# Performance work log

Hardware: AMD Instinct MI355X
Metric: run time of the kernel (lower is better)

Reference implementation:

```python
import jax, jax.numpy as jnp
from jax import lax
import numpy as np

D_STATE = 64
BATCH = 64
SEQ_L = 8192


def setup_inputs() -> dict:
    key = jax.random.key(0)
    kx, ka, kb, kc, kd = jax.random.split(key, 5)
    x = jax.random.normal(kx, (BATCH, SEQ_L), dtype=jnp.float32)
    # A = -rand(d_state) - 1.0  -> strictly negative continuous eigenvalues
    A = -jax.random.uniform(ka, (D_STATE,), dtype=jnp.float32) - 1.0
    B = jax.random.normal(kb, (D_STATE, 1), dtype=jnp.float32)
    C = jax.random.normal(kc, (1, D_STATE), dtype=jnp.float32)
    log_delta = jax.random.normal(kd, (1,), dtype=jnp.float32)
    return {"x": x, "A": A, "B": B, "C": C, "log_delta": log_delta}


def reference(x, A, B, C, log_delta):
    batch, L = x.shape
    # --- ZOH discretization ---
    delta = jnp.exp(log_delta)                      # (1,)
    dA = delta * A                                  # (d_state,)  = delta * A
    A_bar = jnp.exp(dA)                             # (d_state,)
    B_bar = ((A_bar - 1.0) / A)[:, None] * B        # (d_state, 1)
    # --- Vandermonde kernel build: K[k] = C @ (A_bar**k * B_bar) ---
    # A_bar**k computed stably as exp(k * delta * A); shape (L, d_state)
    powers = jnp.exp(jnp.arange(L, dtype=x.dtype)[:, None] * dA[None, :])
    K = powers @ (C[0] * B_bar[:, 0])               # (L,)
    # --- Causal convolution: y[t] = sum_{m<=t} K[m] * x[t-m] ---
    # lax.conv is cross-correlation, so the flipped kernel + left padding (L-1)
    # reproduces F.conv1d(x, flip(K), padding=L-1)[..., :L].
    y = lax.conv_general_dilated(
        x[:, None, :],                              # (batch, 1, L)
        K[::-1][None, None, :],                     # (1, 1, L)
        window_strides=(1,),
        padding=[(L - 1, 0)],
        dimension_numbers=("NCH", "OIH", "NCH"),
    )
    return y[:, 0, :]                               # (batch, L)
```

## Files before the change

kernel.cpp:

```cpp
#include <hip/hip_runtime.h>


#define SEQ_L 8192
#define NB    64
#define MCAP  1532
#define XWIN  (1536 + 1024)

__global__ __launch_bounds__(256) void ssm_fir(const float* __restrict__ x,
                                               const float* __restrict__ A,
                                               const float* __restrict__ B,
                                               const float* __restrict__ C,
                                               const float* __restrict__ logd,
                                               float* __restrict__ out)
{
    __shared__ __align__(16) float Kl[1536];
    __shared__ __align__(16) float xL[XWIN];
    __shared__ float sW[64], sDA[64];
    __shared__ int   sM;

    const int tid = threadIdx.x;
    const float delta = __expf(logd[0]);

    if (tid < 64) {
        const float Ad = A[tid];
        const float dA = delta * Ad;
        const float r  = __expf(dA);
        const float w  = C[tid] * (r - 1.f) / Ad * B[tid];
        sW[tid]  = w;
        sDA[tid] = dA;
        float t = fabsf(w) / (1.f - r);
        #pragma unroll
        for (int off = 32; off; off >>= 1) t += __shfl_xor(t, off);
        if (tid == 0) {
            const int M = (int)ceilf((logf(t) + 11.6f) / delta);
            sM = min(max(M, 1), MCAP);
        }
    }
    __syncthreads();
    const int M4 = (sM + 3) & ~3;
    const int H  = (M4 & ~63) + 64;

    for (int mb = tid >> 2; mb < M4; mb += 64) {
        const int d0 = (tid & 3) * 16;
        const float fm = (float)mb;
        float s = 0.f;
        #pragma unroll
        for (int dd = 0; dd < 16; ++dd) {
            const int d = d0 + dd;
            s = fmaf(sW[d], __expf(fm * sDA[d]), s);
        }
        s += __shfl_xor(s, 1);
        s += __shfl_xor(s, 2);
        if ((tid & 3) == 0) Kl[mb] = s;
    }

    const int b  = blockIdx.x >> 3;
    const int t0 = (blockIdx.x & 7) * 1024;
    const float* xb = x + b * SEQ_L;
    const int n4 = (H + 1024) >> 2;
    for (int s4 = tid; s4 < n4; s4 += 256) {
        const int t = t0 - H + s4 * 4;
        float4 v = make_float4(0.f, 0.f, 0.f, 0.f);
        if (t >= 0) v = *(const float4*)(xb + t);
        *(float4*)(xL + s4 * 4) = v;
    }
    __syncthreads();

    const int base = H + tid * 4;
    float4 Wlo = *(const float4*)(xL + base - 4);
    float4 Whi = *(const float4*)(xL + base);
    float a0 = 0.f, a1 = 0.f, a2 = 0.f, a3 = 0.f;
    for (int m0 = 0; m0 < M4; m0 += 4) {
        const float4 Kv = *(const float4*)(Kl + m0);
        a0 = fmaf(Kv.x, Whi.x, a0); a1 = fmaf(Kv.x, Whi.y, a1);
        a2 = fmaf(Kv.x, Whi.z, a2); a3 = fmaf(Kv.x, Whi.w, a3);
        a0 = fmaf(Kv.y, Wlo.w, a0); a1 = fmaf(Kv.y, Whi.x, a1);
        a2 = fmaf(Kv.y, Whi.y, a2); a3 = fmaf(Kv.y, Whi.z, a3);
        a0 = fmaf(Kv.z, Wlo.z, a0); a1 = fmaf(Kv.z, Wlo.w, a1);
        a2 = fmaf(Kv.z, Whi.x, a2); a3 = fmaf(Kv.z, Whi.y, a3);
        a0 = fmaf(Kv.w, Wlo.y, a0); a1 = fmaf(Kv.w, Wlo.z, a1);
        a2 = fmaf(Kv.w, Wlo.w, a2); a3 = fmaf(Kv.w, Whi.x, a3);
        Whi = Wlo;
        Wlo = *(const float4*)(xL + base - m0 - 8);
    }
    *(float4*)(out + b * SEQ_L + t0 + tid * 4) = make_float4(a0, a1, a2, a3);
}

extern "C" void kernel_launch(void* const* d_in, const int* in_sizes, int n_in,
                              void* d_out, int out_size, void* d_ws, size_t ws_size,
                              hipStream_t stream) {
    const float* x    = (const float*)d_in[0];
    const float* A    = (const float*)d_in[1];
    const float* B    = (const float*)d_in[2];
    const float* C    = (const float*)d_in[3];
    const float* logd = (const float*)d_in[4];
    float* out = (float*)d_out;

    ssm_fir<<<NB * 8, 256, 0, stream>>>(x, A, B, C, logd, out);
}
```

Baseline: 10.01 us.

## Halve output tile per block and prefetch x window before kernel-tap setup

Each block now produces 512 outputs with 128 threads instead of 1024 outputs with 256 threads, which doubles the grid to 1024 blocks. The x history window is a fixed 1536 samples, and each thread issues its global loads into registers at kernel start so they overlap the discretization and tap computation before being written to shared memory. The cost is that every block recomputes the truncated kernel taps with half as many threads. The fixed window also loads more history than the old adaptive size when M is small.

```diff
diff --git a/kernel.cpp b/kernel.cpp
--- a/kernel.cpp
+++ b/kernel.cpp
@@ -4,9 +4,11 @@
 #define SEQ_L 8192
 #define NB    64
 #define MCAP  1532
-#define XWIN  (1536 + 1024)
+#define HST   1536
+#define OUTB  512
+#define XWIN  (HST + OUTB)
 
-__global__ __launch_bounds__(256) void ssm_fir(const float* __restrict__ x,
+__global__ __launch_bounds__(128) void ssm_fir(const float* __restrict__ x,
                                                const float* __restrict__ A,
                                                const float* __restrict__ B,
                                                const float* __restrict__ C,
@@ -19,8 +21,19 @@
     __shared__ int   sM;
 
     const int tid = threadIdx.x;
+    const int b   = blockIdx.x >> 4;
+    const int t0  = (blockIdx.x & 15) * OUTB;
+    const float* xb = x + b * SEQ_L;
+
+    float4 st[4];
+    #pragma unroll
+    for (int i = 0; i < 4; ++i) {
+        const int t = t0 - HST + (tid + i * 128) * 4;
+        st[i] = make_float4(0.f, 0.f, 0.f, 0.f);
+        if (t >= 0) st[i] = *(const float4*)(xb + t);
+    }
+
     const float delta = __expf(logd[0]);
-
     if (tid < 64) {
         const float Ad = A[tid];
         const float dA = delta * Ad;
@@ -36,37 +49,28 @@
             sM = min(max(M, 1), MCAP);
         }
     }
+
+    #pragma unroll
+    for (int i = 0; i < 4; ++i)
+        *(float4*)(xL + (tid + i * 128) * 4) = st[i];
     __syncthreads();
+
     const int M4 = (sM + 3) & ~3;
-    const int H  = (M4 & ~63) + 64;
 
-    for (int mb = tid >> 2; mb < M4; mb += 64) {
+    for (int mb = tid >> 2; mb < M4; mb += 32) {
         const int d0 = (tid & 3) * 16;
         const float fm = (float)mb;
         float s = 0.f;
         #pragma unroll
-        for (int dd = 0; dd < 16; ++dd) {
-            const int d = d0 + dd;
-            s = fmaf(sW[d], __expf(fm * sDA[d]), s);
-        }
+        for (int dd = 0; dd < 16; ++dd)
+            s = fmaf(sW[d0 + dd], __expf(fm * sDA[d0 + dd]), s);
         s += __shfl_xor(s, 1);
         s += __shfl_xor(s, 2);
         if ((tid & 3) == 0) Kl[mb] = s;
     }
-
-    const int b  = blockIdx.x >> 3;
-    const int t0 = (blockIdx.x & 7) * 1024;
-    const float* xb = x + b * SEQ_L;
-    const int n4 = (H + 1024) >> 2;
-    for (int s4 = tid; s4 < n4; s4 += 256) {
-        const int t = t0 - H + s4 * 4;
-        float4 v = make_float4(0.f, 0.f, 0.f, 0.f);
-        if (t >= 0) v = *(const float4*)(xb + t);
-        *(float4*)(xL + s4 * 4) = v;
-    }
     __syncthreads();
 
-    const int base = H + tid * 4;
+    const int base = HST + tid * 4;
     float4 Wlo = *(const float4*)(xL + base - 4);
     float4 Whi = *(const float4*)(xL + base);
     float a0 = 0.f, a1 = 0.f, a2 = 0.f, a3 = 0.f;
@@ -96,5 +100,5 @@
     const float* logd = (const float*)d_in[4];
     float* out = (float*)d_out;
 
-    ssm_fir<<<NB * 8, 256, 0, stream>>>(x, A, B, C, logd, out);
+    ssm_fir<<<NB * 16, 128, 0, stream>>>(x, A, B, C, logd, out);
 }
```

After: 10.16 us. No clear change (+1.5%).
